# Kernel optimization log

Hardware: AMD Instinct MI355X
Metric: run time of the kernel (lower is better)

## Reference

```python
import jax, jax.numpy as jnp
from jax import lax
import numpy as np

S, B, HP, WP, CIN, CO, DS, DI, K = 6, 1, 37, 37, 1536, 256, 16, 512, 4
N = HP * WP          # 1369 patches (37x37 grid)
OH, OW = 148, 148
HID = max(S * CO // 4, S)  # 384, attention hidden


def setup_inputs() -> dict:
    key = jax.random.key(0)
    ks = iter(jax.random.split(key, 64))
    def nrm(shape, scale):
        return jax.random.normal(next(ks), shape, jnp.float32) * scale
    inp = {}
    inp["features"] = nrm((S, B, 1, N, CIN), 1.0)
    # AdaptiveFusionModule (global branch)
    inp["proj_w"] = nrm((S, CO, CIN), CIN ** -0.5)          # per-source 1x1 conv
    inp["attn_w1"] = nrm((S * CO, HID), (S * CO) ** -0.5)
    inp["attn_b1"] = jnp.zeros((HID,), jnp.float32)
    inp["attn_w2"] = nrm((HID, S), HID ** -0.5)
    inp["attn_b2"] = jnp.zeros((S,), jnp.float32)
    inp["src_scale"] = jnp.ones((S,), jnp.float32)
    # two SelectiveSSM parameter sets (fwd / bwd scan)
    def ssm_params(tag):
        d = {}
        d[tag + "_in_w"] = nrm((CO, 2 * DI), CO ** -0.5)
        d[tag + "_conv_w"] = nrm((K, DI), K ** -0.5)         # depthwise causal conv
        d[tag + "_conv_b"] = jnp.zeros((DI,), jnp.float32)
        d[tag + "_xp_w"] = nrm((DI, 2 * DS + DI + 1), 0.02)  # B, C, delta, dt_bias
        # trained A_log; scaled so the log-domain cumsum stays in fp32 range over L=1369
        d[tag + "_Alog"] = jnp.log(jnp.arange(1, DS + 1, dtype=jnp.float32) / 1000.0) * jnp.ones((DI, 1), jnp.float32)
        d[tag + "_D"] = jnp.ones((DI,), jnp.float32)
        d[tag + "_out_w"] = nrm((DI, CO), DI ** -0.5)
        d[tag + "_ln_g"] = jnp.ones((CO,), jnp.float32)
        d[tag + "_ln_b"] = jnp.zeros((CO,), jnp.float32)
        return d
    inp.update(ssm_params("f"))
    inp.update(ssm_params("b"))
    inp["merge_w"] = nrm((2 * CO, CO), (2 * CO) ** -0.5)     # MSSR merge 1x1 conv
    inp["co1_w"] = nrm((3, 3, CO, CO), (9 * CO) ** -0.5)     # conv_out1, HWIO
    inp["co1_b"] = jnp.zeros((CO,), jnp.float32)
    inp["hp"], inp["wp"], inp["out_h"], inp["out_w"] = HP, WP, OH, OW
    return inp


def _causal_dwconv(z, w, b):
    # z: [B,L,D], w: [K,D] -> torch Conv1d(groups=D, padding=K-1)[..., :L]
    Kk, L = w.shape[0], z.shape[1]
    zp = jnp.pad(z, ((0, 0), (Kk - 1, 0), (0, 0)))
    return sum(zp[:, k:k + L, :] * w[k] for k in range(Kk)) + b


def _ssm(x, in_w, conv_w, conv_b, xp_w, Alog, D, out_w, ln_g, ln_b):
    # x: [B,L,d_model] -> [B,L,d_model]
    z, gate = jnp.split(x @ in_w, 2, axis=-1)               # [B,L,DI] each
    z = jax.nn.silu(_causal_dwconv(z, conv_w, conv_b))
    xp = z @ xp_w                                           # [B,L,2*DS+DI+1]
    ds = Alog.shape[1]
    Bp, Cp = xp[..., :ds], xp[..., ds:2 * ds]
    delta = jax.nn.softplus(xp[..., 2 * ds:-1] + xp[..., -1:])  # [B,L,DI]
    dA = jnp.exp(delta[..., None] * (-jnp.exp(Alog)))       # [B,L,DI,DS]
    dBu = delta[..., None] * Bp[:, :, None, :] * z[..., None]
    # log-domain cumsum scan: h[t] = sum_s exp(cs[t]-cs[s]) * dBu[s]
    cs = jnp.cumsum(jnp.log(jnp.clip(dA, 1e-38)), axis=1)
    h = jnp.exp(cs) * jnp.cumsum(jnp.exp(-cs) * dBu, axis=1)
    y = (h * Cp[:, :, None, :]).sum(-1) + D * z             # [B,L,DI]
    y = (y * jax.nn.silu(gate)) @ out_w                     # [B,L,d_model]
    r = y + x                                               # residual + LayerNorm
    mu = r.mean(-1, keepdims=True)
    v = ((r - mu) ** 2).mean(-1, keepdims=True)
    return ln_g * (r - mu) * lax.rsqrt(v + 1e-5) + ln_b


def _forward(features, proj_w, attn_w1, attn_b1, attn_w2, attn_b2, src_scale,
             f_in_w, f_conv_w, f_conv_b, f_xp_w, f_Alog, f_D, f_out_w, f_ln_g, f_ln_b,
             b_in_w, b_conv_w, b_conv_b, b_xp_w, b_Alog, b_D, b_out_w, b_ln_g, b_ln_b,
             merge_w, co1_w, co1_b, hp, wp, out_h, out_w):
    feats = features[:, :, 0]                               # [S,B,N,Cin]
    pf = jnp.einsum('sbnc,soc->sbno', feats, proj_w)        # [S,B,N,Co] per-source 1x1 proj
    Bsz = pf.shape[1]
    concat = pf.mean(2).transpose(1, 0, 2).reshape(Bsz, -1)  # [B,S*Co] pooled concat
    w = jax.nn.softmax(jax.nn.relu(concat @ attn_w1 + attn_b1) @ attn_w2 + attn_b2, axis=-1)
    w = jax.nn.softmax(w * src_scale, axis=-1)              # double softmax as in torch
    fused = jnp.einsum('bs,sbnc->bnc', w, pf)               # [B,N,Co]
    # MSSR bidirectional scan over row-major flattened patches
    fwd = _ssm(fused, f_in_w, f_conv_w, f_conv_b, f_xp_w, f_Alog, f_D, f_out_w, f_ln_g, f_ln_b)
    bwd = _ssm(fused[:, ::-1], b_in_w, b_conv_w, b_conv_b, b_xp_w, b_Alog, b_D, b_out_w, b_ln_g, b_ln_b)[:, ::-1]
    out = jnp.concatenate([fwd, bwd], axis=-1) @ merge_w    # [B,N,Co]
    sp = out.reshape(Bsz, hp, wp, -1)                       # NHWC
    up = jax.image.resize(sp, (Bsz, out_h, out_w, sp.shape[-1]), method='bilinear')
    y = lax.conv_general_dilated(up, co1_w, (1, 1), 'SAME',
                                 dimension_numbers=('NHWC', 'HWIO', 'NHWC')) + co1_b
    return y.transpose(0, 3, 1, 2)                          # [B,Co,out_h,out_w]


def reference(features, proj_w, attn_w1, attn_b1, attn_w2, attn_b2, src_scale,
              f_in_w, f_conv_w, f_conv_b, f_xp_w, f_Alog, f_D, f_out_w, f_ln_g, f_ln_b,
              b_in_w, b_conv_w, b_conv_b, b_xp_w, b_Alog, b_D, b_out_w, b_ln_g, b_ln_b,
              merge_w, co1_w, co1_b, hp, wp, out_h, out_w):
    return _forward(features, proj_w, attn_w1, attn_b1, attn_w2, attn_b2, src_scale,
                    f_in_w, f_conv_w, f_conv_b, f_xp_w, f_Alog, f_D, f_out_w, f_ln_g, f_ln_b,
                    b_in_w, b_conv_w, b_conv_b, b_xp_w, b_Alog, b_D, b_out_w, b_ln_g, b_ln_b,
                    merge_w, co1_w, co1_b, hp, wp, out_h, out_w)
```

## Files before the change

### kernel.cpp

```cpp
#include <hip/hip_runtime.h>
#include <math.h>


namespace {
constexpr int kS   = 6;
constexpr int kHP  = 37;
constexpr int kWP  = 37;
constexpr int kN   = 1369;
constexpr int kCIN = 1536;
constexpr int kCO  = 256;
constexpr int kDS  = 16;
constexpr int kDI  = 512;
constexpr int kHID = 384;
constexpr int kOH  = 148;
constexpr int kOW  = 148;
constexpr int kNP  = kOH * kOW;
constexpr int kXPW = 545;
constexpr long kXPS = 746112;
constexpr int kNC  = 48;
constexpr int kCH  = 29;

constexpr long OFF_PF      = 0;
constexpr long OFF_Z2B     = 0;
constexpr long OFF_YGB     = 0;
constexpr long OFF_UPB     = 0;
constexpr long OFF_SCANP   = 700928;
constexpr long OFF_SCANH   = 1487360;
constexpr long OFF_COLPART = 2102784;
constexpr long OFF_WFIN    = 2119680;
constexpr long OFF_ATTNP   = 2119696;
constexpr long OFF_PROJWB  = 2200000;
constexpr long OFF_INWT    = 2200000;
constexpr long OFF_FUSEDB  = 2462144;
constexpr long OFF_ZG      = 2820624;
constexpr long OFF_Z       = 5760000;
constexpr long OFF_WCONVB  = 6000000;
constexpr long OFF_FEATB   = 7161856;
constexpr long OFF_XP      = 7161856;
constexpr long OFF_DELTA   = 8654080;
constexpr long OFF_OUTWT   = 10055936;
constexpr long OFF_GT      = 11457792;
constexpr long OFF_XPWT    = 11457792;
constexpr long OFF_FUSED2  = 12158720;
constexpr long OFF_CAT     = 12859648;
constexpr long OFF_MERGEWT = 13210112;
constexpr long OFF_MERGED  = 13560576;
}

typedef __attribute__((ext_vector_type(8))) short bf16x8;
typedef __attribute__((ext_vector_type(4))) float f32x4;

__device__ __forceinline__ short f2bf(float x) {
    unsigned u = __builtin_bit_cast(unsigned, x);
    unsigned r = u + 0x7fffu + ((u >> 16) & 1u);
    return (short)(r >> 16);
}

__device__ __forceinline__ bf16x8 cvt8(float4 x, float4 y) {
    union { short s[8]; bf16x8 v; } u;
    u.s[0] = f2bf(x.x); u.s[1] = f2bf(x.y); u.s[2] = f2bf(x.z); u.s[3] = f2bf(x.w);
    u.s[4] = f2bf(y.x); u.s[5] = f2bf(y.y); u.s[6] = f2bf(y.z); u.s[7] = f2bf(y.w);
    return u.v;
}

__global__ __launch_bounds__(256)
void cast8_kernel(const float* __restrict__ in, short* __restrict__ out, long n8)
{
    long i = (long)blockIdx.x * 256 + threadIdx.x;
    if (i >= n8) return;
    const float4* p = (const float4*)(in + i * 8);
    *(bf16x8*)(out + i * 8) = cvt8(p[0], p[1]);
}

__global__ __launch_bounds__(256)
void transpose_cast_kernel(const float* __restrict__ w0, const float* __restrict__ w1,
                           short* __restrict__ wt, int K, int N)
{
    __shared__ float tile[32][33];
    int dir = blockIdx.z;
    const float* w = dir ? w1 : w0;
    short* o = wt + (long)dir * K * N;
    int k0 = blockIdx.x * 32, n0 = blockIdx.y * 32;
    int tx = threadIdx.x & 31, ty = threadIdx.x >> 5;
    #pragma unroll
    for (int r = 0; r < 32; r += 8) {
        int k = k0 + ty + r, n = n0 + tx;
        tile[ty + r][tx] = (k < K && n < N) ? w[(long)k * N + n] : 0.f;
    }
    __syncthreads();
    #pragma unroll
    for (int r = 0; r < 32; r += 8) {
        int n = n0 + ty + r, k = k0 + tx;
        if (n < N && k < K) o[(long)n * K + k] = f2bf(tile[tx][ty + r]);
    }
}

__global__ __launch_bounds__(256)
void mfma_nt(const short* __restrict__ A, long sA,
             const short* __restrict__ B, long sB,
             float* __restrict__ C, long sC,
             int M, int N, int K)
{
    __shared__ short smem[2][8192];
    const int bz = blockIdx.z;
    const short* Ab = A + (long)bz * sA;
    const short* Bb = B + (long)bz * sB;
    float* Cb = C + (long)bz * sC;
    const int t = threadIdx.x, w = t >> 6, l = t & 63;
    const int lr = l & 15, sg = l >> 4;
    const int m0 = blockIdx.x * 64, n0 = blockIdx.y * 64;

    const int srow = t >> 3, qa = t & 7;
    long gA[2]; int woffA[2];
    #pragma unroll
    for (int j = 0; j < 2; ++j) {
        int ar = srow + j * 32;
        int am = m0 + ar; if (am >= M) am = M - 1;
        gA[j] = (long)am * K + qa * 8;
        woffA[j] = ar * 128 + ((qa ^ (ar & 7)) << 4);
    }
    long gB[2]; int woffB[2];
    #pragma unroll
    for (int j = 0; j < 2; ++j) {
        int br = srow + j * 32;
        int bn = n0 + br; if (bn >= N) bn = N - 1;
        gB[j] = (long)bn * K + qa * 8;
        woffB[j] = 8192 + br * 128 + ((qa ^ (br & 7)) << 4);
    }

    int aoff[2][2], boff[2][2];
    #pragma unroll
    for (int mi = 0; mi < 2; ++mi) {
        int r = (w >> 1) * 32 + mi * 16 + lr;
        #pragma unroll
        for (int kk = 0; kk < 2; ++kk)
            aoff[mi][kk] = r * 128 + (((kk * 4 + sg) ^ (r & 7)) << 4);
    }
    #pragma unroll
    for (int ni = 0; ni < 2; ++ni) {
        int r = (w & 1) * 32 + ni * 16 + lr;
        #pragma unroll
        for (int kk = 0; kk < 2; ++kk)
            boff[ni][kk] = 8192 + r * 128 + (((kk * 4 + sg) ^ (r & 7)) << 4);
    }

    f32x4 acc[2][2] = {};
    const int NT = K >> 6;
    {
        char* lb = (char*)&smem[0][0];
        #pragma unroll
        for (int j = 0; j < 2; ++j)
            *(bf16x8*)(lb + woffA[j]) = *(const bf16x8*)(Ab + gA[j]);
        #pragma unroll
        for (int j = 0; j < 2; ++j)
            *(bf16x8*)(lb + woffB[j]) = *(const bf16x8*)(Bb + gB[j]);
    }
    __syncthreads();
    for (int tt = 0; tt < NT; ++tt) {
        bf16x8 nsa[2], nsb[2];
        if (tt + 1 < NT) {
            long o = (long)(tt + 1) * 64;
            #pragma unroll
            for (int j = 0; j < 2; ++j) nsa[j] = *(const bf16x8*)(Ab + gA[j] + o);
            #pragma unroll
            for (int j = 0; j < 2; ++j) nsb[j] = *(const bf16x8*)(Bb + gB[j] + o);
        }
        char* lb = (char*)&smem[tt & 1][0];
        #pragma unroll
        for (int kk = 0; kk < 2; ++kk) {
            bf16x8 a[2], b[2];
            #pragma unroll
            for (int mi = 0; mi < 2; ++mi) a[mi] = *(const bf16x8*)(lb + aoff[mi][kk]);
            #pragma unroll
            for (int ni = 0; ni < 2; ++ni) b[ni] = *(const bf16x8*)(lb + boff[ni][kk]);
            #pragma unroll
            for (int mi = 0; mi < 2; ++mi)
                #pragma unroll
                for (int ni = 0; ni < 2; ++ni)
                    acc[mi][ni] = __builtin_amdgcn_mfma_f32_16x16x32_bf16(a[mi], b[ni], acc[mi][ni], 0, 0, 0);
        }
        if (tt + 1 < NT) {
            char* nb = (char*)&smem[(tt + 1) & 1][0];
            #pragma unroll
            for (int j = 0; j < 2; ++j) *(bf16x8*)(nb + woffA[j]) = nsa[j];
            #pragma unroll
            for (int j = 0; j < 2; ++j) *(bf16x8*)(nb + woffB[j]) = nsb[j];
        }
        __syncthreads();
    }
    const int q = l >> 4;
    const int wm0 = m0 + (w >> 1) * 32, wn0 = n0 + (w & 1) * 32;
    #pragma unroll
    for (int mi = 0; mi < 2; ++mi)
        #pragma unroll
        for (int ni = 0; ni < 2; ++ni)
            #pragma unroll
            for (int r = 0; r < 4; ++r) {
                int m = wm0 + mi * 16 + q * 4 + r;
                int n = wn0 + ni * 16 + lr;
                if (m < M && n < N)
                    Cb[(long)m * N + n] = acc[mi][ni][r];
            }
}

__global__ __launch_bounds__(256)
void proj_mfma_kernel(const short* __restrict__ Ab16, const short* __restrict__ Bb16,
                      float* __restrict__ pf)
{
    __shared__ short smem[2][8192];
    const int bid = blockIdx.x;
    const int slot = (bid & 7) * 66 + (bid >> 3);
    const int s = slot / 88, rem = slot - s * 88;
    const int m0 = (rem >> 2) * 64, n0 = (rem & 3) * 64;
    const short* A = Ab16 + (long)s * kN * kCIN;
    const short* B = Bb16 + (long)s * kCO * kCIN;
    float* C = pf + (long)s * kN * kCO;
    const int t = threadIdx.x, w = t >> 6, l = t & 63;
    const int lr = l & 15, sg = l >> 4;

    const int srow = t >> 3, qa = t & 7;
    long gA[2]; int woffA[2];
    #pragma unroll
    for (int j = 0; j < 2; ++j) {
        int ar = srow + j * 32;
        int am = m0 + ar; if (am >= kN) am = kN - 1;
        gA[j] = (long)am * kCIN + qa * 8;
        woffA[j] = ar * 128 + ((qa ^ (ar & 7)) << 4);
    }
    long gB[2]; int woffB[2];
    #pragma unroll
    for (int j = 0; j < 2; ++j) {
        int br = srow + j * 32;
        gB[j] = (long)(n0 + br) * kCIN + qa * 8;
        woffB[j] = 8192 + br * 128 + ((qa ^ (br & 7)) << 4);
    }

    int aoff[2][2], boff[2][2];
    #pragma unroll
    for (int mi = 0; mi < 2; ++mi) {
        int r = (w >> 1) * 32 + mi * 16 + lr;
        #pragma unroll
        for (int kk = 0; kk < 2; ++kk)
            aoff[mi][kk] = r * 128 + (((kk * 4 + sg) ^ (r & 7)) << 4);
    }
    #pragma unroll
    for (int ni = 0; ni < 2; ++ni) {
        int r = (w & 1) * 32 + ni * 16 + lr;
        #pragma unroll
        for (int kk = 0; kk < 2; ++kk)
            boff[ni][kk] = 8192 + r * 128 + (((kk * 4 + sg) ^ (r & 7)) << 4);
    }

    f32x4 acc[2][2] = {};
    const int NT = kCIN >> 6;
    {
        char* lb = (char*)&smem[0][0];
        #pragma unroll
        for (int j = 0; j < 2; ++j)
            *(bf16x8*)(lb + woffA[j]) = *(const bf16x8*)(A + gA[j]);
        #pragma unroll
        for (int j = 0; j < 2; ++j)
            *(bf16x8*)(lb + woffB[j]) = *(const bf16x8*)(B + gB[j]);
    }
    __syncthreads();
    for (int tt = 0; tt < NT; ++tt) {
        bf16x8 nsa[2], nsb[2];
        if (tt + 1 < NT) {
            long o = (long)(tt + 1) * 64;
            #pragma unroll
            for (int j = 0; j < 2; ++j) nsa[j] = *(const bf16x8*)(A + gA[j] + o);
            #pragma unroll
            for (int j = 0; j < 2; ++j) nsb[j] = *(const bf16x8*)(B + gB[j] + o);
        }
        char* lb = (char*)&smem[tt & 1][0];
        #pragma unroll
        for (int kk = 0; kk < 2; ++kk) {
            bf16x8 a[2], b[2];
            #pragma unroll
            for (int mi = 0; mi < 2; ++mi) a[mi] = *(const bf16x8*)(lb + aoff[mi][kk]);
            #pragma unroll
            for (int ni = 0; ni < 2; ++ni) b[ni] = *(const bf16x8*)(lb + boff[ni][kk]);
            #pragma unroll
            for (int mi = 0; mi < 2; ++mi)
                #pragma unroll
                for (int ni = 0; ni < 2; ++ni)
                    acc[mi][ni] = __builtin_amdgcn_mfma_f32_16x16x32_bf16(a[mi], b[ni], acc[mi][ni], 0, 0, 0);
        }
        if (tt + 1 < NT) {
            char* nb = (char*)&smem[(tt + 1) & 1][0];
            #pragma unroll
            for (int j = 0; j < 2; ++j) *(bf16x8*)(nb + woffA[j]) = nsa[j];
            #pragma unroll
            for (int j = 0; j < 2; ++j) *(bf16x8*)(nb + woffB[j]) = nsb[j];
        }
        __syncthreads();
    }
    const int q = l >> 4;
    const int wm0 = m0 + (w >> 1) * 32, wn0 = n0 + (w & 1) * 32;
    #pragma unroll
    for (int mi = 0; mi < 2; ++mi)
        #pragma unroll
        for (int ni = 0; ni < 2; ++ni)
            #pragma unroll
            for (int r = 0; r < 4; ++r) {
                int m = wm0 + mi * 16 + q * 4 + r;
                if (m < kN)
                    C[(long)m * kCO + wn0 + ni * 16 + lr] = acc[mi][ni][r];
            }
}

__global__ __launch_bounds__(256)
void conv_mfma_kernel(const short* __restrict__ up, const short* __restrict__ wt,
                      const float* __restrict__ bias, float* __restrict__ out)
{
    __shared__ short smem[2][12288];
    const int t = threadIdx.x, w = t >> 6, l = t & 63;
    const int lr = l & 15, sg = l >> 4;
    const int bid = blockIdx.x;
    const int xcd = bid & 7, slot = bid >> 3;
    const int wgid = (xcd < 6 ? xcd * 86 : 6 * 86 + (xcd - 6) * 85) + slot;
    const int pm0 = (wgid >> 1) * 64;
    const int bn0 = (wgid & 1) * 128;

    const int srow = t >> 3, qa = t & 7;
    long gA[2]; int woffA[2];
    #pragma unroll
    for (int j = 0; j < 2; ++j) {
        int ar = srow + j * 32;
        int p = pm0 + ar; if (p >= kNP) p = kNP - 1;
        int oy = p / kOW, ox = p - oy * kOW;
        gA[j] = ((long)oy * 150 + ox) * kCO + qa * 8;
        woffA[j] = ar * 128 + ((qa ^ (ar & 7)) << 4);
    }
    long gB[4]; int woffB[4];
    #pragma unroll
    for (int j = 0; j < 4; ++j) {
        int br = srow + j * 32;
        gB[j] = (long)(bn0 + br) * 2304 + qa * 8;
        woffB[j] = 8192 + br * 128 + ((qa ^ (br & 7)) << 4);
    }

    int aoff[2][2], boff[4][2];
    #pragma unroll
    for (int mi = 0; mi < 2; ++mi) {
        int r = (w >> 1) * 32 + mi * 16 + lr;
        #pragma unroll
        for (int kk = 0; kk < 2; ++kk)
            aoff[mi][kk] = r * 128 + (((kk * 4 + sg) ^ (r & 7)) << 4);
    }
    #pragma unroll
    for (int ni = 0; ni < 4; ++ni) {
        int r = (w & 1) * 64 + ni * 16 + lr;
        #pragma unroll
        for (int kk = 0; kk < 2; ++kk)
            boff[ni][kk] = 8192 + r * 128 + (((kk * 4 + sg) ^ (r & 7)) << 4);
    }

    f32x4 acc[2][4] = {};
    const int NT = 36;

#define CONV_BAR() { \
        asm volatile("s_waitcnt lgkmcnt(0)" ::: "memory"); \
        __builtin_amdgcn_sched_barrier(0); \
        __builtin_amdgcn_s_barrier(); }

#define CONV_TADDR(tn, ta, tb) { \
        int _tap = (tn) >> 2, _c0 = ((tn) & 3) << 6; \
        int _ky = _tap / 3, _kx = _tap - _ky * 3; \
        ta = ((long)_ky * 150 + _kx) * kCO + _c0; \
        tb = (long)(tn) * 64; }

#define CONV_LOAD(Pa_, Pb_, tn) { \
        long _ta, _tb; CONV_TADDR(tn, _ta, _tb); \
        _Pragma("unroll") \
        for (int j = 0; j < 2; ++j) Pa_[j] = *(const bf16x8*)(up + gA[j] + _ta); \
        _Pragma("unroll") \
        for (int j = 0; j < 4; ++j) Pb_[j] = *(const bf16x8*)(wt + gB[j] + _tb); }

#define CONV_WRITE(buf, Pa_, Pb_) { \
        char* _nb = (char*)&smem[buf][0]; \
        _Pragma("unroll") \
        for (int j = 0; j < 2; ++j) *(bf16x8*)(_nb + woffA[j]) = Pa_[j]; \
        _Pragma("unroll") \
        for (int j = 0; j < 4; ++j) *(bf16x8*)(_nb + woffB[j]) = Pb_[j]; }

#define CONV_COMPUTE(buf) { \
        char* _lb = (char*)&smem[buf][0]; \
        _Pragma("unroll") \
        for (int kk = 0; kk < 2; ++kk) { \
            bf16x8 _a[2], _b[4]; \
            _Pragma("unroll") \
            for (int mi = 0; mi < 2; ++mi) _a[mi] = *(const bf16x8*)(_lb + aoff[mi][kk]); \
            _Pragma("unroll") \
            for (int ni = 0; ni < 4; ++ni) _b[ni] = *(const bf16x8*)(_lb + boff[ni][kk]); \
            __builtin_amdgcn_s_setprio(1); \
            _Pragma("unroll") \
            for (int mi = 0; mi < 2; ++mi) \
                _Pragma("unroll") \
                for (int ni = 0; ni < 4; ++ni) \
                    acc[mi][ni] = __builtin_amdgcn_mfma_f32_16x16x32_bf16(_a[mi], _b[ni], acc[mi][ni], 0, 0, 0); \
            __builtin_amdgcn_s_setprio(0); \
        } }

    bf16x8 PaA[2], PaB[4];
    bf16x8 PbA[2], PbB[4];

    CONV_LOAD(PaA, PaB, 0);
    CONV_WRITE(0, PaA, PaB);
    CONV_LOAD(PbA, PbB, 1);
    CONV_BAR();

    for (int tt = 0; tt < NT; tt += 2) {
        if (tt + 2 < NT) CONV_LOAD(PaA, PaB, tt + 2);
        CONV_COMPUTE(0);
        CONV_WRITE(1, PbA, PbB);
        CONV_BAR();
        if (tt + 3 < NT) CONV_LOAD(PbA, PbB, tt + 3);
        CONV_COMPUTE(1);
        if (tt + 2 < NT) CONV_WRITE(0, PaA, PaB);
        CONV_BAR();
    }
#undef CONV_BAR
#undef CONV_TADDR
#undef CONV_LOAD
#undef CONV_WRITE
#undef CONV_COMPUTE

    const int q = l >> 4;
    const int m0 = pm0 + (w >> 1) * 32;
    const int n0 = bn0 + (w & 1) * 64;
    #pragma unroll
    for (int mi = 0; mi < 2; ++mi)
        #pragma unroll
        for (int ni = 0; ni < 4; ++ni) {
            const int co = n0 + ni * 16 + lr;
            const float bv = bias[co];
            #pragma unroll
            for (int r = 0; r < 4; ++r) {
                int p = m0 + mi * 16 + q * 4 + r;
                if (p < kNP)
                    out[(long)co * kNP + p] = acc[mi][ni][r] + bv;
            }
        }
}

__global__ __launch_bounds__(256)
void colmean_kernel(const float* __restrict__ pf, float* __restrict__ colpart)
{
    int s = blockIdx.x, ch = blockIdx.y, o = threadIdx.x;
    int n0 = ch * 128, n1 = n0 + 128 > kN ? kN : n0 + 128;
    float a = 0.f;
    for (int n = n0; n < n1; ++n) a += pf[((long)s * kN + n) * kCO + o];
    colpart[ch * kS * kCO + s * kCO + o] = a;
}

__global__ __launch_bounds__(384)
void attn_part1(const float* __restrict__ colpart, const float* __restrict__ w1,
                float* __restrict__ partial)
{
    __shared__ float cm[128];
    int b = blockIdx.x, t = threadIdx.x;
    int c0 = b * 128;
    if (t < 128) {
        float a = 0.f;
        #pragma unroll
        for (int ch = 0; ch < 11; ++ch) a += colpart[ch * kS * kCO + c0 + t];
        cm[t] = a * (1.f / kN);
    }
    __syncthreads();
    float acc = 0.f;
    #pragma unroll 4
    for (int c = 0; c < 128; ++c) acc += cm[c] * w1[(long)(c0 + c) * kHID + t];
    partial[b * kHID + t] = acc;
}

__global__ __launch_bounds__(384)
void attn_part2(const float* __restrict__ partial, const float* __restrict__ b1,
                const float* __restrict__ w2, const float* __restrict__ b2,
                const float* __restrict__ ss, float* __restrict__ wfin)
{
    __shared__ float h[kHID];
    __shared__ float logits[8];
    int t = threadIdx.x;
    float acc = b1[t];
    #pragma unroll
    for (int b = 0; b < 12; ++b) acc += partial[b * kHID + t];
    h[t] = fmaxf(acc, 0.f);
    __syncthreads();
    if (t < kS) {
        float lg = b2[t];
        for (int j = 0; j < kHID; ++j) lg += h[j] * w2[j * kS + t];
        logits[t] = lg;
    }
    __syncthreads();
    if (t == 0) {
        float w[kS], mx = -1e30f, sum = 0.f;
        for (int s = 0; s < kS; ++s) mx = fmaxf(mx, logits[s]);
        for (int s = 0; s < kS; ++s) { w[s] = expf(logits[s] - mx); sum += w[s]; }
        for (int s = 0; s < kS; ++s) w[s] /= sum;
        mx = -1e30f;
        for (int s = 0; s < kS; ++s) { w[s] *= ss[s]; mx = fmaxf(mx, w[s]); }
        sum = 0.f;
        float e[kS];
        for (int s = 0; s < kS; ++s) { e[s] = expf(w[s] - mx); sum += e[s]; }
        for (int s = 0; s < kS; ++s) wfin[s] = e[s] / sum;
    }
}

__global__ __launch_bounds__(256)
void fuse_kernel(const float* __restrict__ pf, const float* __restrict__ wfin,
                 float* __restrict__ fused2, short* __restrict__ fusedb2)
{
    long idx = (long)blockIdx.x * 256 + threadIdx.x;
    if (idx >= (long)kN * kCO) return;
    float acc = 0.f;
    #pragma unroll
    for (int s = 0; s < kS; ++s) acc += wfin[s] * pf[(long)s * kN * kCO + idx];
    long n = idx / kCO; int c = (int)(idx % kCO);
    long ridx = (long)kN * kCO + (kN - 1 - n) * kCO + c;
    short bv = f2bf(acc);
    fused2[idx] = acc;
    fused2[ridx] = acc;
    fusedb2[idx] = bv;
    fusedb2[ridx] = bv;
}

__global__ __launch_bounds__(256)
void dwconv_kernel(const float* __restrict__ zg2,
                   const float* __restrict__ wf, const float* __restrict__ bf,
                   const float* __restrict__ wb, const float* __restrict__ bb,
                   float* __restrict__ z2, short* __restrict__ z2b)
{
    long idx = (long)blockIdx.x * 256 + threadIdx.x;
    int dir = blockIdx.y;
    if (idx >= (long)kN * kDI) return;
    long n = idx >> 9; int i = (int)(idx & (kDI - 1));
    const float* zg = zg2 + (long)dir * kN * 2 * kDI;
    const float* w  = dir ? wb : wf;
    const float* b  = dir ? bb : bf;
    float acc = b[i];
    #pragma unroll
    for (int k = 0; k < 4; ++k) {
        long m = n - 3 + k;
        if (m >= 0) acc += w[k * kDI + i] * zg[m * 2 * kDI + i];
    }
    float sg = 1.f / (1.f + expf(-acc));
    float v = acc * sg;
    z2 [(long)dir * kN * kDI + idx] = v;
    z2b[(long)dir * kN * kDI + idx] = f2bf(v);
}

__global__ __launch_bounds__(256)
void delta_kernel(const float* __restrict__ xp2, float* __restrict__ delta2)
{
    long idx = (long)blockIdx.x * 256 + threadIdx.x;
    int dir = blockIdx.y;
    if (idx >= (long)kN * kDI) return;
    long n = idx >> 9; int i = (int)(idx & (kDI - 1));
    const float* xp = xp2 + (long)dir * kXPS + n * kXPW;
    float x = xp[2 * kDS + i] + xp[kXPW - 1];
    float sp = fmaxf(x, 0.f) + log1pf(expf(-fabsf(x)));
    delta2[(long)dir * kN * kDI + idx] = sp;
}

__global__ __launch_bounds__(256)
void scan_partA(const float* __restrict__ delta2, const float* __restrict__ z2,
                const float* __restrict__ xp2,
                const float* __restrict__ Alogf, const float* __restrict__ Alogb,
                float* __restrict__ chunkP, float* __restrict__ chunkH)
{
    int bx = blockIdx.x;
    int c  = blockIdx.y;
    int dir = bx >> 5, iblk = bx & 31;
    int t = threadIdx.x;
    int s = t & 15, il = t >> 4;
    int i = iblk * 16 + il;
    int gid = dir * 8192 + iblk * 256 + t;
    const float* Alog = dir ? Alogb : Alogf;
    float A = expf(Alog[i * kDS + s]);
    int n0 = c * kCH, n1 = n0 + kCH; if (n1 > kN) n1 = kN;
    const int cnt = n1 - n0;
    const float* dp = delta2 + (long)dir * kN * kDI + (long)n0 * kDI + i;
    const float* zp = z2     + (long)dir * kN * kDI + (long)n0 * kDI + i;
    const float* xpp = xp2   + (long)dir * kXPS     + (long)n0 * kXPW;

    float d0 = *dp, v0 = *zp, b0 = xpp[s];
    dp += kDI; zp += kDI; xpp += kXPW;
    float d1 = 0.f, v1 = 0.f, b1 = 0.f;
    if (cnt > 1) { d1 = *dp; v1 = *zp; b1 = xpp[s]; }

    float h = 0.f, P = 1.f;
    for (int k = 0; k < cnt; ++k) {
        dp += kDI; zp += kDI; xpp += kXPW;
        float d2 = 0.f, v2 = 0.f, b2 = 0.f;
        if (k + 2 < cnt) { d2 = *dp; v2 = *zp; b2 = xpp[s]; }
        float dA = __expf(-d0 * A);
        h = dA * h + d0 * b0 * v0;
        P *= dA;
        d0 = d1; v0 = v1; b0 = b1;
        d1 = d2; v1 = v2; b1 = b2;
    }
    chunkP[(long)c * 16384 + gid] = P;
    chunkH[(long)c * 16384 + gid] = h;
}

__global__ __launch_bounds__(256)
void scan_partB(float* __restrict__ chunkP, const float* __restrict__ chunkH)
{
    int gid = blockIdx.x * 256 + threadIdx.x;
    float P0 = chunkP[gid];
    float Q0 = chunkH[gid];
    float P1 = chunkP[16384L + gid];
    float Q1 = chunkH[16384L + gid];
    float H = 0.f;
    for (int c = 0; c < kNC; ++c) {
        float P2 = 0.f, Q2 = 0.f;
        if (c + 2 < kNC) {
            P2 = chunkP[(long)(c + 2) * 16384 + gid];
            Q2 = chunkH[(long)(c + 2) * 16384 + gid];
        }
        chunkP[(long)c * 16384 + gid] = H;
        H = P0 * H + Q0;
        P0 = P1; Q0 = Q1;
        P1 = P2; Q1 = Q2;
    }
}

__global__ __launch_bounds__(256)
void scan_partC(const float* __restrict__ delta2, const float* __restrict__ z2,
                const float* __restrict__ xp2, const float* __restrict__ zg2,
                const float* __restrict__ Df, const float* __restrict__ Db,
                const float* __restrict__ Alogf, const float* __restrict__ Alogb,
                const float* __restrict__ hin, short* __restrict__ ygb)
{
    int bx = blockIdx.x;
    int c  = blockIdx.y;
    int dir = bx >> 5, iblk = bx & 31;
    int t = threadIdx.x;
    int s = t & 15, il = t >> 4;
    int i = iblk * 16 + il;
    int gid = dir * 8192 + iblk * 256 + t;
    const float* D    = dir ? Db : Df;
    const float* Alog = dir ? Alogb : Alogf;
    float A  = expf(Alog[i * kDS + s]);
    float Dv = D[i];
    int n0 = c * kCH, n1 = n0 + kCH; if (n1 > kN) n1 = kN;
    const int cnt = n1 - n0;
    const float* dp  = delta2 + (long)dir * kN * kDI + (long)n0 * kDI + i;
    const float* zp  = z2     + (long)dir * kN * kDI + (long)n0 * kDI + i;
    const float* xpp = xp2    + (long)dir * kXPS     + (long)n0 * kXPW;
    const float* gp  = zg2    + (long)dir * kN * 2 * kDI + (long)n0 * 2 * kDI + kDI + i;
    short* yp        = ygb    + (long)dir * kN * kDI + (long)n0 * kDI + i;

    float d0 = *dp, v0 = *zp, b0 = xpp[s], c0 = xpp[kDS + s];
    float g0 = 0.f; if (s == 0) g0 = *gp;
    dp += kDI; zp += kDI; xpp += kXPW; gp += 2 * kDI;
    float d1 = 0.f, v1 = 0.f, b1 = 0.f, c1 = 0.f, g1 = 0.f;
    if (cnt > 1) {
        d1 = *dp; v1 = *zp; b1 = xpp[s]; c1 = xpp[kDS + s];
        if (s == 0) g1 = *gp;
    }

    float h = hin[(long)c * 16384 + gid];
    for (int k = 0; k < cnt; ++k) {
        dp += kDI; zp += kDI; xpp += kXPW; gp += 2 * kDI;
        float d2 = 0.f, v2 = 0.f, b2 = 0.f, c2 = 0.f, g2 = 0.f;
        if (k + 2 < cnt) {
            d2 = *dp; v2 = *zp; b2 = xpp[s]; c2 = xpp[kDS + s];
            if (s == 0) g2 = *gp;
        }
        float dA = __expf(-d0 * A);
        h = dA * h + d0 * b0 * v0;
        float cc = h * c0;
        cc += __shfl_xor(cc, 1, 16);
        cc += __shfl_xor(cc, 2, 16);
        cc += __shfl_xor(cc, 4, 16);
        cc += __shfl_xor(cc, 8, 16);
        if (s == 0) {
            float sgm = 1.f / (1.f + __expf(-g0));
            float v = (cc + Dv * v0) * g0 * sgm;
            *yp = f2bf(v);
        }
        yp += kDI;
        d0 = d1; v0 = v1; b0 = b1; c0 = c1; g0 = g1;
        d1 = d2; v1 = v2; b1 = b2; c1 = c2; g1 = g2;
    }
}

__global__ __launch_bounds__(256)
void resid_ln_cat_kernel(const float* __restrict__ gt2, const float* __restrict__ x2,
                         const float* __restrict__ gf, const float* __restrict__ betf,
                         const float* __restrict__ gb, const float* __restrict__ betb,
                         short* __restrict__ catb)
{
    int n = blockIdx.x, dir = blockIdx.y, t = threadIdx.x;
    const float* gt = gt2 + ((long)dir * kN + n) * kCO;
    const float* x  = x2  + ((long)dir * kN + n) * kCO;
    const float* g  = dir ? gb : gf;
    const float* be = dir ? betb : betf;
    float r = gt[t] + x[t];
    float s1 = r, s2 = r * r;
    #pragma unroll
    for (int m = 32; m >= 1; m >>= 1) {
        s1 += __shfl_xor(s1, m, 64);
        s2 += __shfl_xor(s2, m, 64);
    }
    __shared__ float red[8];
    int w = t >> 6;
    if ((t & 63) == 0) { red[w] = s1; red[4 + w] = s2; }
    __syncthreads();
    float S1 = red[0] + red[1] + red[2] + red[3];
    float S2 = red[4] + red[5] + red[6] + red[7];
    float mu  = S1 * (1.f / kCO);
    float var = S2 * (1.f / kCO) - mu * mu;
    float inv = rsqrtf(var + 1e-5f);
    float v = g[t] * (r - mu) * inv + be[t];
    int row = dir ? (kN - 1 - n) : n;
    catb[(long)row * (2 * kCO) + dir * kCO + t] = f2bf(v);
}

__global__ __launch_bounds__(256)
void upsample_kernel(const float* __restrict__ merged, short* __restrict__ up)
{
    int p = blockIdx.x;
    int y = p / 150, x = p - y * 150;
    int c = threadIdx.x;
    if (y == 0 || y == 149 || x == 0 || x == 149) {
        up[((long)y * 150 + x) * kCO + c] = 0;
        return;
    }
    int oy = y - 1, ox = x - 1;
    float sy = (oy + 0.5f) * ((float)kHP / (float)kOH) - 0.5f;
    float sx = (ox + 0.5f) * ((float)kWP / (float)kOW) - 0.5f;
    int iy0 = (int)floorf(sy); float fy = sy - (float)iy0;
    int ix0 = (int)floorf(sx); float fx = sx - (float)ix0;
    float wy0 = 1.f - fy, wy1 = fy, wx0 = 1.f - fx, wx1 = fx;
    int iy1 = iy0 + 1, ix1 = ix0 + 1;
    if (iy0 < 0)       { iy0 = 0;       wy0 = 0.f; }
    if (iy1 > kHP - 1) { iy1 = kHP - 1; wy1 = 0.f; }
    if (ix0 < 0)       { ix0 = 0;       wx0 = 0.f; }
    if (ix1 > kWP - 1) { ix1 = kWP - 1; wx1 = 0.f; }
    float wys = wy0 + wy1; wy0 /= wys; wy1 /= wys;
    float wxs = wx0 + wx1; wx0 /= wxs; wx1 /= wxs;
    const float* M00 = merged + (long)(iy0 * kWP + ix0) * kCO;
    const float* M01 = merged + (long)(iy0 * kWP + ix1) * kCO;
    const float* M10 = merged + (long)(iy1 * kWP + ix0) * kCO;
    const float* M11 = merged + (long)(iy1 * kWP + ix1) * kCO;
    float v = wy0 * (wx0 * M00[c] + wx1 * M01[c]) + wy1 * (wx0 * M10[c] + wx1 * M11[c]);
    up[((long)y * 150 + x) * kCO + c] = f2bf(v);
}

extern "C" void kernel_launch(void* const* d_in, const int* in_sizes, int n_in,
                              void* d_out, int out_size, void* d_ws, size_t ws_size,
                              hipStream_t stream)
{
    (void)in_sizes; (void)n_in; (void)out_size; (void)ws_size;
    const float* features  = (const float*)d_in[0];
    const float* proj_w    = (const float*)d_in[1];
    const float* attn_w1   = (const float*)d_in[2];
    const float* attn_b1   = (const float*)d_in[3];
    const float* attn_w2   = (const float*)d_in[4];
    const float* attn_b2   = (const float*)d_in[5];
    const float* src_scale = (const float*)d_in[6];
    const float* f_in_w    = (const float*)d_in[7];
    const float* f_conv_w  = (const float*)d_in[8];
    const float* f_conv_b  = (const float*)d_in[9];
    const float* f_xp_w    = (const float*)d_in[10];
    const float* f_Alog    = (const float*)d_in[11];
    const float* f_D       = (const float*)d_in[12];
    const float* f_out_w   = (const float*)d_in[13];
    const float* f_ln_g    = (const float*)d_in[14];
    const float* f_ln_b    = (const float*)d_in[15];
    const float* b_in_w    = (const float*)d_in[16];
    const float* b_conv_w  = (const float*)d_in[17];
    const float* b_conv_b  = (const float*)d_in[18];
    const float* b_xp_w    = (const float*)d_in[19];
    const float* b_Alog    = (const float*)d_in[20];
    const float* b_D       = (const float*)d_in[21];
    const float* b_out_w   = (const float*)d_in[22];
    const float* b_ln_g    = (const float*)d_in[23];
    const float* b_ln_b    = (const float*)d_in[24];
    const float* merge_w   = (const float*)d_in[25];
    const float* co1_w     = (const float*)d_in[26];
    const float* co1_b     = (const float*)d_in[27];

    float* ws      = (float*)d_ws;
    float* outp    = (float*)d_out;
    float* pf      = ws + OFF_PF;
    float* colpart = ws + OFF_COLPART;
    float* wfin    = ws + OFF_WFIN;
    float* attnp   = ws + OFF_ATTNP;
    float* fused2  = ws + OFF_FUSED2;
    float* zg2     = ws + OFF_ZG;
    float* z2      = ws + OFF_Z;
    float* xp2     = ws + OFF_XP;
    float* delta2  = ws + OFF_DELTA;
    float* gt2     = ws + OFF_GT;
    float* merged  = ws + OFF_MERGED;
    float* chunkP  = ws + OFF_SCANP;
    float* chunkH  = ws + OFF_SCANH;
    short* featb   = (short*)(ws + OFF_FEATB);
    short* projwb  = (short*)(ws + OFF_PROJWB);
    short* in_wt   = (short*)(ws + OFF_INWT);
    short* xp_wt   = (short*)(ws + OFF_XPWT);
    short* out_wt  = (short*)(ws + OFF_OUTWT);
    short* mrg_wt  = (short*)(ws + OFF_MERGEWT);
    short* fusedb2 = (short*)(ws + OFF_FUSEDB);
    short* z2b     = (short*)(ws + OFF_Z2B);
    short* ygb     = (short*)(ws + OFF_YGB);
    short* catb    = (short*)(ws + OFF_CAT);
    short* upb     = (short*)(ws + OFF_UPB);
    short* wconvb  = (short*)(ws + OFF_WCONVB);

    cast8_kernel<<<dim3(6161), 256, 0, stream>>>(features, featb, 1577088L);
    cast8_kernel<<<dim3(1152), 256, 0, stream>>>(proj_w, projwb, 294912L);
    proj_mfma_kernel<<<dim3(528), 256, 0, stream>>>(featb, projwb, pf);
    transpose_cast_kernel<<<dim3(8, 32, 2), 256, 0, stream>>>(f_in_w, b_in_w, in_wt, 256, 1024);
    transpose_cast_kernel<<<dim3(16, 18, 2), 256, 0, stream>>>(f_xp_w, b_xp_w, xp_wt, 512, 545);
    transpose_cast_kernel<<<dim3(16, 8, 1), 256, 0, stream>>>(merge_w, merge_w, mrg_wt, 512, 256);
    colmean_kernel<<<dim3(6, 11), 256, 0, stream>>>(pf, colpart);
    attn_part1<<<dim3(12), 384, 0, stream>>>(colpart, attn_w1, attnp);
    attn_part2<<<1, 384, 0, stream>>>(attnp, attn_b1, attn_w2, attn_b2, src_scale, wfin);
    fuse_kernel<<<dim3(1369), 256, 0, stream>>>(pf, wfin, fused2, fusedb2);
    transpose_cast_kernel<<<dim3(16, 8, 2), 256, 0, stream>>>(f_out_w, b_out_w, out_wt, 512, 256);
    mfma_nt<<<dim3(22, 16, 2), 256, 0, stream>>>(
        fusedb2, (long)kN * kCO, in_wt, (long)2 * kDI * kCO,
        zg2, (long)kN * 2 * kDI, kN, 2 * kDI, kCO);
    dwconv_kernel<<<dim3(2738, 2), 256, 0, stream>>>(zg2, f_conv_w, f_conv_b,
                                                     b_conv_w, b_conv_b, z2, z2b);
    mfma_nt<<<dim3(22, 9, 2), 256, 0, stream>>>(
        z2b, (long)kN * kDI, xp_wt, (long)kXPW * kDI,
        xp2, kXPS, kN, kXPW, kDI);
    delta_kernel<<<dim3(2738, 2), 256, 0, stream>>>(xp2, delta2);
    scan_partA<<<dim3(64, kNC), 256, 0, stream>>>(delta2, z2, xp2, f_Alog, b_Alog,
                                                  chunkP, chunkH);
    scan_partB<<<dim3(64), 256, 0, stream>>>(chunkP, chunkH);
    scan_partC<<<dim3(64, kNC), 256, 0, stream>>>(delta2, z2, xp2, zg2, f_D, b_D,
                                                  f_Alog, b_Alog, chunkP, ygb);
    mfma_nt<<<dim3(22, 4, 2), 256, 0, stream>>>(
        ygb, (long)kN * kDI, out_wt, (long)kCO * kDI,
        gt2, (long)kN * kCO, kN, kCO, kDI);
    resid_ln_cat_kernel<<<dim3(1369, 2), 256, 0, stream>>>(gt2, fused2, f_ln_g, f_ln_b,
                                                           b_ln_g, b_ln_b, catb);
    mfma_nt<<<dim3(22, 4, 1), 256, 0, stream>>>(
        catb, 0, mrg_wt, 0,
        merged, 0, kN, kCO, 2 * kCO);
    transpose_cast_kernel<<<dim3(72, 8, 1), 256, 0, stream>>>(co1_w, co1_w, wconvb, 2304, 256);
    upsample_kernel<<<dim3(150 * 150), 256, 0, stream>>>(merged, upb);
    conv_mfma_kernel<<<dim3(686), 256, 0, stream>>>(upb, wconvb, co1_b, outp);
}
```

Before: 281.8 us.

## Load conv A operand fragments directly from global into registers, bypassing LDS

```diff
diff --git a/kernel.cpp b/kernel.cpp
--- a/kernel.cpp
+++ b/kernel.cpp
@@ -313,7 +313,7 @@
 void conv_mfma_kernel(const short* __restrict__ up, const short* __restrict__ wt,
                       const float* __restrict__ bias, float* __restrict__ out)
 {
-    __shared__ short smem[2][12288];
+    __shared__ short smem[2][8192];
     const int t = threadIdx.x, w = t >> 6, l = t & 63;
     const int lr = l & 15, sg = l >> 4;
     const int bid = blockIdx.x;
@@ -321,39 +321,32 @@
     const int wgid = (xcd < 6 ? xcd * 86 : 6 * 86 + (xcd - 6) * 85) + slot;
     const int pm0 = (wgid >> 1) * 64;
     const int bn0 = (wgid & 1) * 128;
+    const int wr = w >> 1, wc = w & 1;
+
+    long gAF[2];
+    #pragma unroll
+    for (int mi = 0; mi < 2; ++mi) {
+        int p = pm0 + wr * 32 + mi * 16 + lr; if (p >= kNP) p = kNP - 1;
+        int oy = p / kOW, ox = p - oy * kOW;
+        gAF[mi] = ((long)oy * 150 + ox) * kCO + sg * 8;
+    }
 
     const int srow = t >> 3, qa = t & 7;
-    long gA[2]; int woffA[2];
-    #pragma unroll
-    for (int j = 0; j < 2; ++j) {
-        int ar = srow + j * 32;
-        int p = pm0 + ar; if (p >= kNP) p = kNP - 1;
-        int oy = p / kOW, ox = p - oy * kOW;
-        gA[j] = ((long)oy * 150 + ox) * kCO + qa * 8;
-        woffA[j] = ar * 128 + ((qa ^ (ar & 7)) << 4);
-    }
     long gB[4]; int woffB[4];
     #pragma unroll
     for (int j = 0; j < 4; ++j) {
         int br = srow + j * 32;
         gB[j] = (long)(bn0 + br) * 2304 + qa * 8;
-        woffB[j] = 8192 + br * 128 + ((qa ^ (br & 7)) << 4);
-    }
-
-    int aoff[2][2], boff[4][2];
-    #pragma unroll
-    for (int mi = 0; mi < 2; ++mi) {
-        int r = (w >> 1) * 32 + mi * 16 + lr;
+        woffB[j] = br * 128 + ((qa ^ (br & 7)) << 4);
+    }
+
+    int boff[4][2];
+    #pragma unroll
+    for (int ni = 0; ni < 4; ++ni) {
+        int r = wc * 64 + ni * 16 + lr;
         #pragma unroll
         for (int kk = 0; kk < 2; ++kk)
-            aoff[mi][kk] = r * 128 + (((kk * 4 + sg) ^ (r & 7)) << 4);
-    }
-    #pragma unroll
-    for (int ni = 0; ni < 4; ++ni) {
-        int r = (w & 1) * 64 + ni * 16 + lr;
-        #pragma unroll
-        for (int kk = 0; kk < 2; ++kk)
-            boff[ni][kk] = 8192 + r * 128 + (((kk * 4 + sg) ^ (r & 7)) << 4);
+            boff[ni][kk] = r * 128 + (((kk * 4 + sg) ^ (r & 7)) << 4);
     }
 
     f32x4 acc[2][4] = {};
@@ -370,27 +363,29 @@
         ta = ((long)_ky * 150 + _kx) * kCO + _c0; \
         tb = (long)(tn) * 64; }
 
-#define CONV_LOAD(Pa_, Pb_, tn) { \
-        long _ta, _tb; CONV_TADDR(tn, _ta, _tb); \
-        _Pragma("unroll") \
-        for (int j = 0; j < 2; ++j) Pa_[j] = *(const bf16x8*)(up + gA[j] + _ta); \
+#define CONV_LOADB(Pb_, tn) { \
+        long _ta, _tb; CONV_TADDR(tn, _ta, _tb); (void)_ta; \
         _Pragma("unroll") \
         for (int j = 0; j < 4; ++j) Pb_[j] = *(const bf16x8*)(wt + gB[j] + _tb); }
 
-#define CONV_WRITE(buf, Pa_, Pb_) { \
+#define CONV_LOADA(F_, tn) { \
+        long _ta, _tb; CONV_TADDR(tn, _ta, _tb); (void)_tb; \
+        _Pragma("unroll") \
+        for (int mi = 0; mi < 2; ++mi) \
+            _Pragma("unroll") \
+            for (int kk = 0; kk < 2; ++kk) \
+                F_[mi][kk] = *(const bf16x8*)(up + gAF[mi] + _ta + kk * 32); }
+
+#define CONV_WRITEB(buf, Pb_) { \
         char* _nb = (char*)&smem[buf][0]; \
         _Pragma("unroll") \
-        for (int j = 0; j < 2; ++j) *(bf16x8*)(_nb + woffA[j]) = Pa_[j]; \
-        _Pragma("unroll") \
         for (int j = 0; j < 4; ++j) *(bf16x8*)(_nb + woffB[j]) = Pb_[j]; }
 
-#define CONV_COMPUTE(buf) { \
+#define CONV_COMPUTE(buf, F_) { \
         char* _lb = (char*)&smem[buf][0]; \
         _Pragma("unroll") \
         for (int kk = 0; kk < 2; ++kk) { \
-            bf16x8 _a[2], _b[4]; \
-            _Pragma("unroll") \
-            for (int mi = 0; mi < 2; ++mi) _a[mi] = *(const bf16x8*)(_lb + aoff[mi][kk]); \
+            bf16x8 _b[4]; \
             _Pragma("unroll") \
             for (int ni = 0; ni < 4; ++ni) _b[ni] = *(const bf16x8*)(_lb + boff[ni][kk]); \
             __builtin_amdgcn_s_setprio(1); \
@@ -398,37 +393,41 @@
             for (int mi = 0; mi < 2; ++mi) \
                 _Pragma("unroll") \
                 for (int ni = 0; ni < 4; ++ni) \
-                    acc[mi][ni] = __builtin_amdgcn_mfma_f32_16x16x32_bf16(_a[mi], _b[ni], acc[mi][ni], 0, 0, 0); \
+                    acc[mi][ni] = __builtin_amdgcn_mfma_f32_16x16x32_bf16(F_[mi][kk], _b[ni], acc[mi][ni], 0, 0, 0); \
             __builtin_amdgcn_s_setprio(0); \
         } }
 
-    bf16x8 PaA[2], PaB[4];
-    bf16x8 PbA[2], PbB[4];
-
-    CONV_LOAD(PaA, PaB, 0);
-    CONV_WRITE(0, PaA, PaB);
-    CONV_LOAD(PbA, PbB, 1);
+    bf16x8 PaB[4], PbB[4];
+    bf16x8 FaA[2][2], FbA[2][2];
+
+    CONV_LOADB(PbB, 0);
+    CONV_WRITEB(0, PbB);
+    CONV_LOADB(PaB, 1);
+    CONV_LOADA(FaA, 0);
     CONV_BAR();
 
     for (int tt = 0; tt < NT; tt += 2) {
-        if (tt + 2 < NT) CONV_LOAD(PaA, PaB, tt + 2);
-        CONV_COMPUTE(0);
-        CONV_WRITE(1, PbA, PbB);
+        if (tt + 2 < NT) CONV_LOADB(PbB, tt + 2);
+        CONV_LOADA(FbA, tt + 1);
+        CONV_COMPUTE(0, FaA);
+        CONV_WRITEB(1, PaB);
         CONV_BAR();
-        if (tt + 3 < NT) CONV_LOAD(PbA, PbB, tt + 3);
-        CONV_COMPUTE(1);
-        if (tt + 2 < NT) CONV_WRITE(0, PaA, PaB);
+        if (tt + 3 < NT) CONV_LOADB(PaB, tt + 3);
+        if (tt + 2 < NT) CONV_LOADA(FaA, tt + 2);
+        CONV_COMPUTE(1, FbA);
+        if (tt + 2 < NT) CONV_WRITEB(0, PbB);
         CONV_BAR();
     }
 #undef CONV_BAR
 #undef CONV_TADDR
-#undef CONV_LOAD
-#undef CONV_WRITE
+#undef CONV_LOADB
+#undef CONV_LOADA
+#undef CONV_WRITEB
 #undef CONV_COMPUTE
 
     const int q = l >> 4;
-    const int m0 = pm0 + (w >> 1) * 32;
-    const int n0 = bn0 + (w & 1) * 64;
+    const int m0 = pm0 + wr * 32;
+    const int n0 = bn0 + wc * 64;
     #pragma unroll
     for (int mi = 0; mi < 2; ++mi)
         #pragma unroll
```

Measured after the change: 312.1 us. 1.11x slower.
